# Optimization experiments

Measured on AMD Instinct MI355X. Metric: run time of the kernel, lower is better.

## Reference

```python
import jax, jax.numpy as jnp
import numpy as np


def setup_inputs() -> dict:
    key = jax.random.key(0)
    k1, k2, k3 = jax.random.split(key, 3)
    B, C, H, W = 8, 256, 128, 128
    x = jax.random.normal(k1, (B, C, H, W), dtype=jnp.float32)
    # 1x1 conv: Conv2d(5C -> C), weight stored as [C_out, 5C]
    fan_in = 5 * C
    bound = 1.0 / np.sqrt(fan_in)
    conv_w = jax.random.uniform(k2, (C, 5 * C), dtype=jnp.float32, minval=-bound, maxval=bound)
    conv_b = jax.random.uniform(k3, (C,), dtype=jnp.float32, minval=-bound, maxval=bound)
    return {"x": x, "conv_w": conv_w, "conv_b": conv_b}


def reference(x, conv_w, conv_b):
    # Directional prefix/suffix max.
    # up_to_bottom: cumulative max along H (top->bottom)
    x1 = jax.lax.cummax(x, axis=2)
    # bottom_to_up: suffix max along H
    x2 = jax.lax.cummax(x, axis=2, reverse=True)
    # left_to_right (rot90 trick in torch) == cumulative max along W
    x3 = jax.lax.cummax(x, axis=3)
    # right_to_left == suffix max along W
    x4 = jax.lax.cummax(x, axis=3, reverse=True)
    x_con = jnp.concatenate((x, x1, x2, x3, x4), axis=1)  # [B, 5C, H, W]
    # 1x1 conv == channel contraction
    out = jnp.einsum('bchw,oc->bohw', x_con, conv_w) + conv_b[None, :, None, None]
    return out
```

## Files before the change

kernel.cpp:

```cpp
#include <hip/hip_runtime.h>
#include <stdint.h>


#define N_  131072
#define K_  1280

typedef unsigned short ushort8v __attribute__((ext_vector_type(8)));
typedef unsigned short ushort4v __attribute__((ext_vector_type(4)));
typedef short          short8v  __attribute__((ext_vector_type(8)));
typedef float          float4v  __attribute__((ext_vector_type(4)));

__device__ __forceinline__ unsigned short f2bf(float f) {
    unsigned int u = __builtin_bit_cast(unsigned int, f);
    u += 0x7fffu + ((u >> 16) & 1u);
    return (unsigned short)(u >> 16);
}

__device__ __forceinline__ void load_lds16(const void* g, void* l) {
    __builtin_amdgcn_global_load_lds(
        (const __attribute__((address_space(1))) uint32_t*)g,
        (__attribute__((address_space(3))) uint32_t*)l,
        16, 0, 0);
}

#define WTV(n) asm volatile("s_waitcnt vmcnt(" #n ")" ::: "memory")

__global__ void repack_w(const float* __restrict__ w, unsigned short* __restrict__ wsA) {
    int idx = blockIdx.x * 256 + threadIdx.x;
    float4 v = ((const float4*)w)[idx];
    int m = idx / 320;
    int k = (idx - m * 320) << 2;
    ushort4v o = { f2bf(v.x), f2bf(v.y), f2bf(v.z), f2bf(v.w) };
    *(ushort4v*)(wsA + ((size_t)(k >> 3) << 11) + (m << 3) + (k & 7)) = o;
}

__global__ __launch_bounds__(256) void scan_h(const float* __restrict__ x,
                                              unsigned short* __restrict__ wsB) {
    int idx = blockIdx.x;
    int wq = idx & 3, cb = (idx >> 2) & 31, b = idx >> 7;
    int t = threadIdx.x;
    int w0 = t >> 6, lane = t & 63;
    int c = t >> 5, wi = t & 31;

    __shared__ float xs[8 * 128 * 32];
    __shared__ unsigned short sm0[16 * 32 * 8];
    __shared__ unsigned short sm1[16 * 32 * 8];

    const float* xb = x + (((size_t)(b * 256 + cb * 8)) << 14) + wq * 32;

    {
        int hh = lane >> 3, w4 = lane & 7;
#pragma unroll
        for (int r = 0; r < 32; ++r) {
            int cc = (w0 << 1) + (r & 1);
            int h0 = (r >> 1) << 3;
            const float* g = xb + ((size_t)cc << 14) + (size_t)(h0 + hh) * 128 + (w4 << 2);
            load_lds16(g, (char*)(xs + ((cc << 7) + h0) * 32) + lane * 16);
        }
    }

    unsigned short* d0 = wsB + (((size_t)(cb)      * N_) << 3);
    unsigned short* d1 = wsB + (((size_t)(32 + cb) * N_) << 3);
    unsigned short* d2 = wsB + (((size_t)(64 + cb) * N_) << 3);
    size_t nbase = ((size_t)b << 14) + wq * 32;

    float r = -INFINITY;
#pragma unroll
    for (int hb = 0; hb < 8; ++hb) {
        if      (hb == 0) WTV(28);
        else if (hb == 1) WTV(24);
        else if (hb == 2) WTV(20);
        else if (hb == 3) WTV(16);
        else if (hb == 4) WTV(12);
        else if (hb == 5) WTV(8);
        else if (hb == 6) WTV(4);
        else              WTV(0);
        __builtin_amdgcn_sched_barrier(0);
        int h0 = hb << 4;
#pragma unroll
        for (int hh = 0; hh < 16; ++hh) {
            float v = xs[((c << 7) + h0 + hh) * 32 + wi];
            r = fmaxf(r, v);
            sm0[(((hh << 5) + wi) << 3) + c] = f2bf(v);
            sm1[(((hh << 5) + wi) << 3) + c] = f2bf(r);
        }
        __syncthreads();
#pragma unroll
        for (int k = 0; k < 2; ++k) {
            int p = t + (k << 8);
            int hh = p >> 5, wo = p & 31;
            size_t n = nbase + (size_t)(h0 + hh) * 128 + wo;
            *(ushort8v*)(d0 + (n << 3)) = *(const ushort8v*)(sm0 + (((hh << 5) + wo) << 3));
            *(ushort8v*)(d1 + (n << 3)) = *(const ushort8v*)(sm1 + (((hh << 5) + wo) << 3));
        }
        __syncthreads();
    }

    r = -INFINITY;
#pragma unroll
    for (int hb = 7; hb >= 0; --hb) {
        int h0 = hb << 4;
#pragma unroll
        for (int hh = 15; hh >= 0; --hh) {
            float v = xs[((c << 7) + h0 + hh) * 32 + wi];
            r = fmaxf(r, v);
            sm0[(((hh << 5) + wi) << 3) + c] = f2bf(r);
        }
        __syncthreads();
#pragma unroll
        for (int k = 0; k < 2; ++k) {
            int p = t + (k << 8);
            int hh = p >> 5, wo = p & 31;
            size_t n = nbase + (size_t)(h0 + hh) * 128 + wo;
            *(ushort8v*)(d2 + (n << 3)) = *(const ushort8v*)(sm0 + (((hh << 5) + wo) << 3));
        }
        __syncthreads();
    }
}

__global__ __launch_bounds__(256) void scan_w(const float* __restrict__ x,
                                              unsigned short* __restrict__ wsB) {
    int idx = blockIdx.x;
    int hq = idx & 3, cb = (idx >> 2) & 31, b = idx >> 7;
    int t = threadIdx.x;
    int w0 = t >> 6, lane = t & 63;
    int c = t & 7, h = t >> 3;

    __shared__ float xs[256 * 128];
    __shared__ unsigned short po[16 * 32 * 8];

    const float* xb = x + (((size_t)(b * 256 + cb * 8)) << 14) + ((size_t)(hq * 32) << 7);

    {
        int rsel = lane >> 5, gp = lane & 31;
#pragma unroll
        for (int r = 0; r < 32; ++r) {
            int cc  = r >> 2;
            int rs0 = (cc << 5) + (w0 << 3) + ((r & 3) << 1);
            int row = rs0 + rsel;
            int gl  = gp ^ (row & 7);
            const float* g = xb + ((size_t)cc << 14) + ((size_t)(row & 31) << 7) + (gl << 2);
            load_lds16(g, (char*)(xs + (rs0 << 7)) + lane * 16);
        }
    }
    WTV(0);
    __builtin_amdgcn_sched_barrier(0);

    unsigned short* d3 = wsB + (((size_t)(96  + cb) * N_) << 3);
    unsigned short* d4 = wsB + (((size_t)(128 + cb) * N_) << 3);
    size_t nrow0 = ((size_t)b << 14) + (size_t)(hq * 32) * 128;
    int rs = (c << 5) + h;
    int sw = rs & 7;

    {
        float rr = -INFINITY;
#pragma unroll
        for (int wc = 0; wc < 8; ++wc) {
#pragma unroll
            for (int g = 0; g < 4; ++g) {
                int l = (wc << 2) + g;
                float4v v = *(const float4v*)(xs + (rs << 7) + ((l ^ sw) << 2));
#pragma unroll
                for (int e = 0; e < 4; ++e) {
                    rr = fmaxf(rr, v[e]);
                    int wloc = (g << 2) + e;
                    int G = (wloc << 5) + h;
                    po[((G ^ (wloc & 7)) << 3) + c] = f2bf(rr);
                }
            }
            __syncthreads();
#pragma unroll
            for (int k = 0; k < 2; ++k) {
                int p = t + (k << 8);
                int ww = p & 15, hh = p >> 4;
                int G = (ww << 5) + hh;
                size_t n = nrow0 + (size_t)hh * 128 + (wc << 4) + ww;
                *(ushort8v*)(d3 + (n << 3)) = *(const ushort8v*)(po + ((G ^ (ww & 7)) << 3));
            }
            __syncthreads();
        }
    }
    {
        float rr = -INFINITY;
#pragma unroll
        for (int wc = 7; wc >= 0; --wc) {
#pragma unroll
            for (int g = 3; g >= 0; --g) {
                int l = (wc << 2) + g;
                float4v v = *(const float4v*)(xs + (rs << 7) + ((l ^ sw) << 2));
#pragma unroll
                for (int e = 3; e >= 0; --e) {
                    rr = fmaxf(rr, v[e]);
                    int wloc = (g << 2) + e;
                    int G = (wloc << 5) + h;
                    po[((G ^ (wloc & 7)) << 3) + c] = f2bf(rr);
                }
            }
            __syncthreads();
#pragma unroll
            for (int k = 0; k < 2; ++k) {
                int p = t + (k << 8);
                int ww = p & 15, hh = p >> 4;
                int G = (ww << 5) + hh;
                size_t n = nrow0 + (size_t)hh * 128 + (wc << 4) + ww;
                *(ushort8v*)(d4 + (n << 3)) = *(const ushort8v*)(po + ((G ^ (ww & 7)) << 3));
            }
            __syncthreads();
        }
    }
}


__device__ __forceinline__ void stage_tile(
    const unsigned short* __restrict__ wsA, const unsigned short* __restrict__ wsB,
    int t, int n0, unsigned short* As, unsigned short* Bs, int tid) {
    const unsigned short* ga = wsA + ((((size_t)t << 11) + tid) << 3);
#pragma unroll
    for (int r = 0; r < 4; ++r)
        load_lds16(ga + (r << 12), As + (((r << 9) + tid) << 3));
    int kb0 = t << 3;
#pragma unroll
    for (int r = 0; r < 4; ++r) {
        int idx = (r << 9) + tid;
        load_lds16(wsB + (((size_t)(kb0 + (idx >> 8)) * N_ + n0 + (idx & 255)) << 3),
                   Bs + ((size_t)idx << 3));
    }
}

__device__ __forceinline__ void compute_tile(
    const unsigned short* __restrict__ Ab, const unsigned short* __restrict__ Bb,
    int wr, int wc, int q, int lr, float4v (&acc)[8][4]) {
#pragma unroll
    for (int h = 0; h < 2; ++h) {
        short8v a[8], bb[4];
        int kq = (h << 2) + q;
#pragma unroll
        for (int mi = 0; mi < 8; ++mi)
            a[mi] = *(const short8v*)(Ab + (((kq << 8) + (wr << 7) + (mi << 4) + lr) << 3));
#pragma unroll
        for (int ni = 0; ni < 4; ++ni)
            bb[ni] = *(const short8v*)(Bb + (((kq << 8) + (wc << 6) + (ni << 4) + lr) << 3));
        __builtin_amdgcn_s_setprio(1);
#pragma unroll
        for (int mi = 0; mi < 8; ++mi)
#pragma unroll
            for (int ni = 0; ni < 4; ++ni)
                acc[mi][ni] = __builtin_amdgcn_mfma_f32_16x16x32_bf16(a[mi], bb[ni], acc[mi][ni], 0, 0, 0);
        __builtin_amdgcn_s_setprio(0);
    }
}

__global__ __launch_bounds__(512, 2) void gemm_k(
    const unsigned short* __restrict__ wsA, const unsigned short* __restrict__ wsB,
    const float* __restrict__ bias, float* __restrict__ out) {
    __shared__ __align__(16) unsigned short As[2][16384];
    __shared__ __align__(16) unsigned short Bs[2][16384];

    int tid  = threadIdx.x;
    int lane = tid & 63, wid = tid >> 6;
    int wr = wid >> 2, wc = wid & 3;
    int q  = lane >> 4, lr = lane & 15;
    int bid = blockIdx.x;
    int n0 = (((bid & 7) << 6) + (bid >> 3)) << 8;

    float4v acc[8][4];
#pragma unroll
    for (int mi = 0; mi < 8; ++mi)
#pragma unroll
        for (int ni = 0; ni < 4; ++ni)
            acc[mi][ni] = (float4v){0.f, 0.f, 0.f, 0.f};

    stage_tile(wsA, wsB, 0, n0, As[0], Bs[0], tid);
    stage_tile(wsA, wsB, 1, n0, As[1], Bs[1], tid);
    asm volatile("s_waitcnt vmcnt(8)" ::: "memory");
    __builtin_amdgcn_s_barrier();
    __builtin_amdgcn_sched_barrier(0);

#pragma unroll 1
    for (int t = 0; t < 18; t += 2) {
        compute_tile(As[0], Bs[0], wr, wc, q, lr, acc);
        __builtin_amdgcn_s_barrier();
        __builtin_amdgcn_sched_barrier(0);
        stage_tile(wsA, wsB, t + 2, n0, As[0], Bs[0], tid);
        __builtin_amdgcn_sched_barrier(0);
        asm volatile("s_waitcnt vmcnt(8)" ::: "memory");
        __builtin_amdgcn_s_barrier();
        __builtin_amdgcn_sched_barrier(0);

        compute_tile(As[1], Bs[1], wr, wc, q, lr, acc);
        __builtin_amdgcn_s_barrier();
        __builtin_amdgcn_sched_barrier(0);
        stage_tile(wsA, wsB, t + 3, n0, As[1], Bs[1], tid);
        __builtin_amdgcn_sched_barrier(0);
        asm volatile("s_waitcnt vmcnt(8)" ::: "memory");
        __builtin_amdgcn_s_barrier();
        __builtin_amdgcn_sched_barrier(0);
    }
    compute_tile(As[0], Bs[0], wr, wc, q, lr, acc);
    __builtin_amdgcn_s_barrier();
    asm volatile("s_waitcnt vmcnt(0)" ::: "memory");
    __builtin_amdgcn_s_barrier();
    __builtin_amdgcn_sched_barrier(0);
    compute_tile(As[1], Bs[1], wr, wc, q, lr, acc);

#pragma unroll
    for (int mi = 0; mi < 8; ++mi) {
        int rowb = (wr << 7) + (mi << 4) + (q << 2);
#pragma unroll
        for (int ni = 0; ni < 4; ++ni) {
            int col = n0 + (wc << 6) + (ni << 4) + lr;
            int b   = col >> 14, p = col & 16383;
            float* op = out + ((size_t)((b << 8) + rowb) << 14) + p;
#pragma unroll
            for (int r = 0; r < 4; ++r)
                op[(size_t)r << 14] = acc[mi][ni][r] + bias[rowb + r];
        }
    }
}

extern "C" void kernel_launch(void* const* d_in, const int* in_sizes, int n_in,
                              void* d_out, int out_size, void* d_ws, size_t ws_size,
                              hipStream_t stream) {
    const float* x  = (const float*)d_in[0];
    const float* cw = (const float*)d_in[1];
    const float* cb = (const float*)d_in[2];
    float* out = (float*)d_out;

    unsigned short* wsA = (unsigned short*)d_ws;
    unsigned short* wsB = wsA + 327680;

    repack_w<<<320, 256, 0, stream>>>(cw, wsA);
    scan_h<<<1024, 256, 0, stream>>>(x, wsB);
    scan_w<<<1024, 256, 0, stream>>>(x, wsB);
    gemm_k<<<dim3(512), 512, 0, stream>>>(wsA, wsB, cb, out);
}
```

Before: 439.5 us.

## Stream H-scan from registers, store W-scan input as bf16, double-buffer LDS staging

scan_h no longer stages the whole fp32 tile in LDS. It loads 16 rows per thread into registers, prefetches the next block, and double-buffers the bf16 transpose buffers so one barrier per block replaces two. scan_w converts x to bf16 while loading into LDS, which halves its LDS footprint and can raise occupancy. It also scans on bf16 values and double-buffers its output staging. The scan results are unchanged, since the max of bf16-rounded values equals the bf16 rounding of the max, but the sync pattern is more delicate and the direct global loads lose the async LDS path.

Measured after the change: 427.3 us. 2.8% less time.

```diff
diff --git a/kernel.cpp b/kernel.cpp
--- a/kernel.cpp
+++ b/kernel.cpp
@@ -9,6 +9,8 @@
 typedef unsigned short ushort4v __attribute__((ext_vector_type(4)));
 typedef short          short8v  __attribute__((ext_vector_type(8)));
 typedef float          float4v  __attribute__((ext_vector_type(4)));
+typedef unsigned int   uint2v   __attribute__((ext_vector_type(2)));
+typedef unsigned int   uint4v   __attribute__((ext_vector_type(4)));
 
 __device__ __forceinline__ unsigned short f2bf(float f) {
     unsigned int u = __builtin_bit_cast(unsigned int, f);
@@ -24,6 +26,11 @@
 }
 
 #define WTV(n) asm volatile("s_waitcnt vmcnt(" #n ")" ::: "memory")
+#define LGKM_BAR() do { \
+    asm volatile("s_waitcnt lgkmcnt(0)" ::: "memory"); \
+    __builtin_amdgcn_s_barrier(); \
+    __builtin_amdgcn_sched_barrier(0); \
+} while (0)
 
 __global__ void repack_w(const float* __restrict__ w, unsigned short* __restrict__ wsA) {
     int idx = blockIdx.x * 256 + threadIdx.x;
@@ -39,82 +46,77 @@
     int idx = blockIdx.x;
     int wq = idx & 3, cb = (idx >> 2) & 31, b = idx >> 7;
     int t = threadIdx.x;
-    int w0 = t >> 6, lane = t & 63;
-    int c = t >> 5, wi = t & 31;
-
-    __shared__ float xs[8 * 128 * 32];
-    __shared__ unsigned short sm0[16 * 32 * 8];
-    __shared__ unsigned short sm1[16 * 32 * 8];
-
-    const float* xb = x + (((size_t)(b * 256 + cb * 8)) << 14) + wq * 32;
-
-    {
-        int hh = lane >> 3, w4 = lane & 7;
-#pragma unroll
-        for (int r = 0; r < 32; ++r) {
-            int cc = (w0 << 1) + (r & 1);
-            int h0 = (r >> 1) << 3;
-            const float* g = xb + ((size_t)cc << 14) + (size_t)(h0 + hh) * 128 + (w4 << 2);
-            load_lds16(g, (char*)(xs + ((cc << 7) + h0) * 32) + lane * 16);
-        }
-    }
+    int j = t >> 5, wi = t & 31;
+    const float* src = x + (((size_t)(b * 256 + cb * 8 + j)) << 14) + wq * 32 + wi;
+
+    __shared__ unsigned short sm0[2][4096];
+    __shared__ unsigned short sm1[2][4096];
 
     unsigned short* d0 = wsB + (((size_t)(cb)      * N_) << 3);
     unsigned short* d1 = wsB + (((size_t)(32 + cb) * N_) << 3);
     unsigned short* d2 = wsB + (((size_t)(64 + cb) * N_) << 3);
     size_t nbase = ((size_t)b << 14) + wq * 32;
 
-    float r = -INFINITY;
-#pragma unroll
-    for (int hb = 0; hb < 8; ++hb) {
-        if      (hb == 0) WTV(28);
-        else if (hb == 1) WTV(24);
-        else if (hb == 2) WTV(20);
-        else if (hb == 3) WTV(16);
-        else if (hb == 4) WTV(12);
-        else if (hb == 5) WTV(8);
-        else if (hb == 6) WTV(4);
-        else              WTV(0);
-        __builtin_amdgcn_sched_barrier(0);
-        int h0 = hb << 4;
-#pragma unroll
-        for (int hh = 0; hh < 16; ++hh) {
-            float v = xs[((c << 7) + h0 + hh) * 32 + wi];
-            r = fmaxf(r, v);
-            sm0[(((hh << 5) + wi) << 3) + c] = f2bf(v);
-            sm1[(((hh << 5) + wi) << 3) + c] = f2bf(r);
-        }
-        __syncthreads();
-#pragma unroll
-        for (int k = 0; k < 2; ++k) {
-            int p = t + (k << 8);
-            int hh = p >> 5, wo = p & 31;
-            size_t n = nbase + (size_t)(h0 + hh) * 128 + wo;
-            *(ushort8v*)(d0 + (n << 3)) = *(const ushort8v*)(sm0 + (((hh << 5) + wo) << 3));
-            *(ushort8v*)(d1 + (n << 3)) = *(const ushort8v*)(sm1 + (((hh << 5) + wo) << 3));
-        }
-        __syncthreads();
-    }
-
-    r = -INFINITY;
-#pragma unroll
-    for (int hb = 7; hb >= 0; --hb) {
-        int h0 = hb << 4;
-#pragma unroll
-        for (int hh = 15; hh >= 0; --hh) {
-            float v = xs[((c << 7) + h0 + hh) * 32 + wi];
-            r = fmaxf(r, v);
-            sm0[(((hh << 5) + wi) << 3) + c] = f2bf(r);
-        }
-        __syncthreads();
-#pragma unroll
-        for (int k = 0; k < 2; ++k) {
-            int p = t + (k << 8);
-            int hh = p >> 5, wo = p & 31;
-            size_t n = nbase + (size_t)(h0 + hh) * 128 + wo;
-            *(ushort8v*)(d2 + (n << 3)) = *(const ushort8v*)(sm0 + (((hh << 5) + wo) << 3));
-        }
-        __syncthreads();
+    float v[16];
+    {
+        float r = -INFINITY;
+#pragma unroll
+        for (int hh = 0; hh < 16; ++hh) v[hh] = src[(size_t)hh << 7];
+#pragma unroll
+        for (int hb = 0; hb < 8; ++hb) {
+            int p = hb & 1;
+            int h0 = hb << 4;
+#pragma unroll
+            for (int hh = 0; hh < 16; ++hh) {
+                float vv = v[hh];
+                r = fmaxf(r, vv);
+                sm0[p][(((hh << 5) + wi) << 3) + j] = f2bf(vv);
+                sm1[p][(((hh << 5) + wi) << 3) + j] = f2bf(r);
+            }
+            if (hb < 7) {
+                int h0n = (hb + 1) << 4;
+#pragma unroll
+                for (int hh = 0; hh < 16; ++hh) v[hh] = src[(size_t)(h0n + hh) << 7];
+            }
+            LGKM_BAR();
+#pragma unroll
+            for (int k = 0; k < 2; ++k) {
+                int pp = t + (k << 8);
+                int hh = pp >> 5, wo = pp & 31;
+                size_t n = nbase + (size_t)(h0 + hh) * 128 + wo;
+                *(ushort8v*)(d0 + (n << 3)) = *(const ushort8v*)(&sm0[p][((hh << 5) + wo) << 3]);
+                *(ushort8v*)(d1 + (n << 3)) = *(const ushort8v*)(&sm1[p][((hh << 5) + wo) << 3]);
+            }
+        }
+    }
+    LGKM_BAR();
+    {
+        float r = -INFINITY;
+#pragma unroll
+        for (int hh = 0; hh < 16; ++hh) v[hh] = src[(size_t)(112 + hh) << 7];
+#pragma unroll
+        for (int hb = 7; hb >= 0; --hb) {
+            int p = hb & 1;
+            int h0 = hb << 4;
+#pragma unroll
+            for (int hh = 15; hh >= 0; --hh) {
+                r = fmaxf(r, v[hh]);
+                sm0[p][(((hh << 5) + wi) << 3) + j] = f2bf(r);
+            }
+            if (hb > 0) {
+                int h0n = (hb - 1) << 4;
+#pragma unroll
+                for (int hh = 0; hh < 16; ++hh) v[hh] = src[(size_t)(h0n + hh) << 7];
+            }
+            LGKM_BAR();
+#pragma unroll
+            for (int k = 0; k < 2; ++k) {
+                int pp = t + (k << 8);
+                int hh = pp >> 5, wo = pp & 31;
+                size_t n = nbase + (size_t)(h0 + hh) * 128 + wo;
+                *(ushort8v*)(d2 + (n << 3)) = *(const ushort8v*)(&sm0[p][((hh << 5) + wo) << 3]);
+            }
+        }
     }
 }
 
@@ -123,61 +125,64 @@
     int idx = blockIdx.x;
     int hq = idx & 3, cb = (idx >> 2) & 31, b = idx >> 7;
     int t = threadIdx.x;
-    int w0 = t >> 6, lane = t & 63;
-    int c = t & 7, h = t >> 3;
-
-    __shared__ float xs[256 * 128];
-    __shared__ unsigned short po[16 * 32 * 8];
+
+    __shared__ unsigned short xs[256 * 128];
+    __shared__ unsigned short po[2][4096];
 
     const float* xb = x + (((size_t)(b * 256 + cb * 8)) << 14) + ((size_t)(hq * 32) << 7);
 
-    {
-        int rsel = lane >> 5, gp = lane & 31;
-#pragma unroll
-        for (int r = 0; r < 32; ++r) {
-            int cc  = r >> 2;
-            int rs0 = (cc << 5) + (w0 << 3) + ((r & 3) << 1);
-            int row = rs0 + rsel;
-            int gl  = gp ^ (row & 7);
-            const float* g = xb + ((size_t)cc << 14) + ((size_t)(row & 31) << 7) + (gl << 2);
-            load_lds16(g, (char*)(xs + (rs0 << 7)) + lane * 16);
-        }
-    }
-    WTV(0);
-    __builtin_amdgcn_sched_barrier(0);
+#pragma unroll
+    for (int rr = 0; rr < 32; ++rr) {
+        int f   = (rr << 8) + t;
+        int row = f >> 5, q = f & 31;
+        float4 vv = *(const float4*)(xb + ((size_t)(row >> 5) << 14) +
+                                     ((row & 31) << 7) + (q << 2));
+        uint2v u;
+        u[0] = (unsigned int)f2bf(vv.x) | ((unsigned int)f2bf(vv.y) << 16);
+        u[1] = (unsigned int)f2bf(vv.z) | ((unsigned int)f2bf(vv.w) << 16);
+        int g = q >> 1, half = q & 1;
+        int phys = g ^ (row & 7);
+        *(uint2v*)((char*)xs + row * 256 + phys * 16 + half * 8) = u;
+    }
+    LGKM_BAR();
 
     unsigned short* d3 = wsB + (((size_t)(96  + cb) * N_) << 3);
     unsigned short* d4 = wsB + (((size_t)(128 + cb) * N_) << 3);
     size_t nrow0 = ((size_t)b << 14) + (size_t)(hq * 32) * 128;
+    int c = t & 7, h = t >> 3;
     int rs = (c << 5) + h;
     int sw = rs & 7;
+    int pb = 0;
 
     {
         float rr = -INFINITY;
 #pragma unroll
         for (int wc = 0; wc < 8; ++wc) {
 #pragma unroll
-            for (int g = 0; g < 4; ++g) {
-                int l = (wc << 2) + g;
-                float4v v = *(const float4v*)(xs + (rs << 7) + ((l ^ sw) << 2));
-#pragma unroll
-                for (int e = 0; e < 4; ++e) {
-                    rr = fmaxf(rr, v[e]);
-                    int wloc = (g << 2) + e;
+            for (int g2 = 0; g2 < 2; ++g2) {
+                int g = (wc << 1) + g2;
+                uint4v u = *(const uint4v*)((const char*)xs + rs * 256 + ((g ^ sw) << 4));
+#pragma unroll
+                for (int e = 0; e < 8; ++e) {
+                    unsigned int w32 = u[e >> 1];
+                    unsigned int bits = (e & 1) ? (w32 & 0xffff0000u) : (w32 << 16);
+                    rr = fmaxf(rr, __builtin_bit_cast(float, bits));
+                    int wloc = (g2 << 3) + e;
                     int G = (wloc << 5) + h;
-                    po[((G ^ (wloc & 7)) << 3) + c] = f2bf(rr);
+                    po[pb][((G ^ (wloc & 7)) << 3) + c] =
+                        (unsigned short)(__builtin_bit_cast(unsigned int, rr) >> 16);
                 }
             }
-            __syncthreads();
+            LGKM_BAR();
 #pragma unroll
             for (int k = 0; k < 2; ++k) {
                 int p = t + (k << 8);
                 int ww = p & 15, hh = p >> 4;
                 int G = (ww << 5) + hh;
                 size_t n = nrow0 + (size_t)hh * 128 + (wc << 4) + ww;
-                *(ushort8v*)(d3 + (n << 3)) = *(const ushort8v*)(po + ((G ^ (ww & 7)) << 3));
-            }
-            __syncthreads();
+                *(ushort8v*)(d3 + (n << 3)) = *(const ushort8v*)(&po[pb][(G ^ (ww & 7)) << 3]);
+            }
+            pb ^= 1;
         }
     }
     {
@@ -185,27 +190,30 @@
 #pragma unroll
         for (int wc = 7; wc >= 0; --wc) {
 #pragma unroll
-            for (int g = 3; g >= 0; --g) {
-                int l = (wc << 2) + g;
-                float4v v = *(const float4v*)(xs + (rs << 7) + ((l ^ sw) << 2));
-#pragma unroll
-                for (int e = 3; e >= 0; --e) {
-                    rr = fmaxf(rr, v[e]);
-                    int wloc = (g << 2) + e;
+            for (int g2 = 1; g2 >= 0; --g2) {
+                int g = (wc << 1) + g2;
+                uint4v u = *(const uint4v*)((const char*)xs + rs * 256 + ((g ^ sw) << 4));
+#pragma unroll
+                for (int e = 7; e >= 0; --e) {
+                    unsigned int w32 = u[e >> 1];
+                    unsigned int bits = (e & 1) ? (w32 & 0xffff0000u) : (w32 << 16);
+                    rr = fmaxf(rr, __builtin_bit_cast(float, bits));
+                    int wloc = (g2 << 3) + e;
                     int G = (wloc << 5) + h;
-                    po[((G ^ (wloc & 7)) << 3) + c] = f2bf(rr);
+                    po[pb][((G ^ (wloc & 7)) << 3) + c] =
+                        (unsigned short)(__builtin_bit_cast(unsigned int, rr) >> 16);
                 }
             }
-            __syncthreads();
+            LGKM_BAR();
 #pragma unroll
             for (int k = 0; k < 2; ++k) {
                 int p = t + (k << 8);
                 int ww = p & 15, hh = p >> 4;
                 int G = (ww << 5) + hh;
                 size_t n = nrow0 + (size_t)hh * 128 + (wc << 4) + ww;
-                *(ushort8v*)(d4 + (n << 3)) = *(const ushort8v*)(po + ((G ^ (ww & 7)) << 3));
-            }
-            __syncthreads();
+                *(ushort8v*)(d4 + (n << 3)) = *(const ushort8v*)(&po[pb][(G ^ (ww & 7)) << 3]);
+            }
+            pb ^= 1;
         }
     }
 }
```
